# Kernel optimization log

Hardware: AMD Instinct MI355X
Metric: run time of the kernel (lower is better)

The kernel has to match this reference:

```python
import jax, jax.numpy as jnp
import numpy as np

B, N, K, F, E = 2, 16384, 32, 64, 16


def setup_inputs() -> dict:
    key = jax.random.key(0)
    k1, k2, k3, k4 = jax.random.split(key, 4)
    nodes = jax.random.normal(k1, (B, N, F), dtype=jnp.float32)
    # neighbor list: for each (batch, node) a list of K neighbor node indices
    nlist = jax.random.randint(k2, (B, N, K), 0, N, dtype=jnp.int32)
    edges = jax.random.normal(k3, (B, N, K, E), dtype=jnp.float32)
    # learned weight: (node_feat, node_feat, edge_feat) as in build()
    w = jax.random.normal(k4, (F, F, E), dtype=jnp.float32) * 0.05
    return {"nodes": nodes, "nlist": nlist, "edges": edges, "w": w}


def reference(nodes, nlist, edges, w):
    # tf.gather_nd(nodes, nlist): gather neighbor features -> [B, N, K, F]
    batch_idx = jnp.arange(nodes.shape[0], dtype=nlist.dtype)[:, None, None]
    sliced = nodes[batch_idx, nlist]  # [B, N, K, F]
    # edge-conditioned contraction: edges[b,i,j,n] * sliced[b,i,j,l] * w[l,m,n]
    prod = jnp.einsum('bijn,bijl,lmn->bijm', edges, sliced, w)  # [B, N, K, F]
    # mean over the K neighbors (axis=2); activation is None
    reduced = jnp.mean(prod, axis=2)  # [B, N, F]
    return reduced
```

## Files before the change

kernel.cpp:

```cpp
#include <hip/hip_runtime.h>
#include <cstdint>
#include <cstddef>

#define LOGN 14

typedef __bf16 bf16x8 __attribute__((ext_vector_type(8)));
typedef float f32x4 __attribute__((ext_vector_type(4)));
typedef unsigned u32;

#define BARRIER() __builtin_amdgcn_s_barrier()
#define LGKM0()   __builtin_amdgcn_s_waitcnt(0xC07F)
#define SFENCE()  __builtin_amdgcn_sched_barrier(0)

__device__ __forceinline__ u32 fbits(float f) { return __builtin_bit_cast(u32, f); }
__device__ __forceinline__ u32 pkrne(float lo, float hi) {
  u32 a = fbits(lo); a = a + 0x7fffu + ((a >> 16) & 1u);
  u32 b = fbits(hi); b = b + 0x7fffu + ((b >> 16) & 1u);
  return (b & 0xffff0000u) | (a >> 16);
}

__global__ void prep_wt(const float* __restrict__ w, unsigned short* __restrict__ wt) {
  int idx = blockIdx.x * 256 + threadIdx.x;
  int m = idx >> 10, k = idx & 1023, l = k >> 4, n = k & 15;
  u32 u = fbits(w[l * 1024 + m * 16 + n] * 0.03125f);
  wt[idx] = (unsigned short)((u + 0x7fffu + ((u >> 16) & 1u)) >> 16);
}

__device__ __forceinline__ bf16x8 mk_bw(const float* wp) {
  float v[8];
  #pragma unroll
  for (int i = 0; i < 8; ++i) v[i] = wp[i] * 0.03125f;
  uint4 pk{pkrne(v[0], v[1]), pkrne(v[2], v[3]), pkrne(v[4], v[5]), pkrne(v[6], v[7])};
  return __builtin_bit_cast(bf16x8, pk);
}

template <bool USE_WT>
__global__ __launch_bounds__(256, 3)
void mp_kernel(const float* __restrict__ nodes, const int* __restrict__ nlist,
               const float* __restrict__ edges, const unsigned short* __restrict__ wt,
               const float* __restrict__ w, float* __restrict__ out) {
  __shared__ u32 g_lds[16 * 512];

  const int tid = threadIdx.x;
  const int lane = tid & 63;
  const int wid = __builtin_amdgcn_readfirstlane(tid >> 6);
  const int q = lane >> 4, c = lane & 15;

  const int blk = blockIdx.x;
  const int xcd = blk & 7;
  const int batch = xcd >> 2;
  const int ordinal = ((blk >> 3) << 2) + (xcd & 3);
  const int wg0 = (batch << LOGN) + (ordinal << 4);
  const float* __restrict__ nbase = nodes + ((size_t)batch << 20);

  const int nd0 = wid << 2;

  auto issue_nl = [&](int t, int4* ni) {
    const int* r = nlist + (((size_t)(wg0 + nd0 + t)) << 5) + (q << 3);
    ni[0] = *(const int4*)r;
    ni[1] = *(const int4*)(r + 4);
  };
  auto issue_se = [&](int t, const int4* ni, float* S, float* E) {
    const int ix[8] = {ni[0].x, ni[0].y, ni[0].z, ni[0].w,
                       ni[1].x, ni[1].y, ni[1].z, ni[1].w};
    #pragma unroll
    for (int i = 0; i < 8; ++i) {
      const float* rp = nbase + ((size_t)(u32)ix[i] << 6) + c;
      #pragma unroll
      for (int lt = 0; lt < 4; ++lt) S[i * 4 + lt] = rp[lt << 4];
    }
    const float* ep = edges + (((size_t)(wg0 + nd0 + t)) << 9) + (q << 7) + c;
    #pragma unroll
    for (int i = 0; i < 8; ++i) E[i] = ep[i << 4];
  };
  auto consume = [&](int p, const float* S, const float* E) {
    uint4 apk{pkrne(E[0], E[1]), pkrne(E[2], E[3]),
              pkrne(E[4], E[5]), pkrne(E[6], E[7])};
    const bf16x8 af = __builtin_bit_cast(bf16x8, apk);
    #pragma unroll
    for (int lt = 0; lt < 4; ++lt) {
      uint4 spk{pkrne(S[0 * 4 + lt], S[1 * 4 + lt]),
                pkrne(S[2 * 4 + lt], S[3 * 4 + lt]),
                pkrne(S[4 * 4 + lt], S[5 * 4 + lt]),
                pkrne(S[6 * 4 + lt], S[7 * 4 + lt])};
      f32x4 acc{0.f, 0.f, 0.f, 0.f};
      acc = __builtin_amdgcn_mfma_f32_16x16x32_bf16(af,
              __builtin_bit_cast(bf16x8, spk), acc, 0, 0, 0);
      const u32 lo = pkrne(acc[0], acc[1]);
      const u32 hi = pkrne(acc[2], acc[3]);
      const int chunk = ((((lt << 4) + c) << 1) + (q >> 1)) ^ (p & 7);
      *(uint2*)&g_lds[(p << 9) + (chunk << 2) + ((q & 1) << 1)] = uint2{lo, hi};
    }
  };

  {
    int4 ni0[2], ni1[2];
    float S0[32], E0[8], S1[32], E1[8];
    issue_nl(0, ni0);
    issue_nl(1, ni1);
    issue_se(0, ni0, S0, E0);
    issue_nl(2, ni0);
    issue_se(1, ni1, S1, E1);
    issue_nl(3, ni1);
    SFENCE();
    consume(nd0 + 0, S0, E0);
    issue_se(2, ni0, S0, E0);
    SFENCE();
    consume(nd0 + 1, S1, E1);
    issue_se(3, ni1, S1, E1);
    SFENCE();
    consume(nd0 + 2, S0, E0);
    consume(nd0 + 3, S1, E1);
  }

  LGKM0();
  BARRIER();

  const int m = (wid << 4) + c;
  f32x4 ob{0.f, 0.f, 0.f, 0.f};
  if (USE_WT) {
    const unsigned short* wb = wt + ((size_t)m << 10) + (q << 3);
    #pragma unroll 8
    for (int s = 0; s < 32; ++s) {
      uint4 ar = *(const uint4*)&g_lds[(c << 9) + ((((s << 2) + q) ^ (c & 7)) << 2)];
      ob = __builtin_amdgcn_mfma_f32_16x16x32_bf16(__builtin_bit_cast(bf16x8, ar),
                                                   *(const bf16x8*)(wb + (s << 5)),
                                                   ob, 0, 0, 0);
    }
  } else {
    #pragma unroll 4
    for (int s = 0; s < 32; ++s) {
      uint4 ar = *(const uint4*)&g_lds[(c << 9) + ((((s << 2) + q) ^ (c & 7)) << 2)];
      const int l = 2 * s + (q >> 1);
      const float* wp = w + l * 1024 + m * 16 + ((q & 1) << 3);
      ob = __builtin_amdgcn_mfma_f32_16x16x32_bf16(__builtin_bit_cast(bf16x8, ar),
                                                   mk_bw(wp), ob, 0, 0, 0);
    }
  }

  #pragma unroll
  for (int r = 0; r < 4; ++r)
    out[((size_t)(wg0 + (q << 2) + r) << 6) + m] = ob[r];
}

extern "C" void kernel_launch(void* const* d_in, const int* in_sizes, int n_in,
                              void* d_out, int out_size, void* d_ws, size_t ws_size,
                              hipStream_t stream) {
  const float* nodes = (const float*)d_in[0];
  const int*   nlist = (const int*)d_in[1];
  const float* edges = (const float*)d_in[2];
  const float* w     = (const float*)d_in[3];
  float* out = (float*)d_out;

  if (ws_size >= 131072) {
    unsigned short* wt = (unsigned short*)d_ws;
    prep_wt<<<256, 256, 0, stream>>>(w, wt);
    mp_kernel<true><<<2048, 256, 0, stream>>>(nodes, nlist, edges, wt, w, out);
  } else {
    mp_kernel<false><<<2048, 256, 0, stream>>>(nodes, nlist, edges, nullptr, w, out);
  }
}
```

Measured before the change: 147.6 us.

## Vectorize neighbor feature gather to float4 and permute feature-to-lane mapping

Each lane now loads four contiguous features per neighbor with a single 16-byte load, replacing four strided scalar loads per neighbor. This changes which feature index each lane owns, so the LDS chunk layout of the intermediate and the weight reordering in both the prep kernel and the fallback path are permuted to match. The aim is fewer, wider gather loads with better coalescing per row, at the cost of a more intricate index mapping that has to stay consistent across all three places.

Measured after the change: 148.1 us. Within noise of the previous version (+0.3%).

```diff
diff --git a/kernel.cpp b/kernel.cpp
--- a/kernel.cpp
+++ b/kernel.cpp
@@ -19,9 +19,12 @@
   return (b & 0xffff0000u) | (a >> 16);
 }
 
+
 __global__ void prep_wt(const float* __restrict__ w, unsigned short* __restrict__ wt) {
   int idx = blockIdx.x * 256 + threadIdx.x;
-  int m = idx >> 10, k = idx & 1023, l = k >> 4, n = k & 15;
+  int m = idx >> 10, k = idx & 1023;
+  int ch = k >> 3, wv = k & 7, t = ch >> 4, cc = ch & 15;
+  int l = (cc << 2) + (t >> 1), n = ((t & 1) << 3) + wv;
   u32 u = fbits(w[l * 1024 + m * 16 + n] * 0.03125f);
   wt[idx] = (unsigned short)((u + 0x7fffu + ((u >> 16) & 1u)) >> 16);
 }
@@ -60,57 +63,53 @@
     ni[0] = *(const int4*)r;
     ni[1] = *(const int4*)(r + 4);
   };
-  auto issue_se = [&](int t, const int4* ni, float* S, float* E) {
+  auto issue_se = [&](int t, const int4* ni, f32x4* R, float* E) {
     const int ix[8] = {ni[0].x, ni[0].y, ni[0].z, ni[0].w,
                        ni[1].x, ni[1].y, ni[1].z, ni[1].w};
     #pragma unroll
-    for (int i = 0; i < 8; ++i) {
-      const float* rp = nbase + ((size_t)(u32)ix[i] << 6) + c;
-      #pragma unroll
-      for (int lt = 0; lt < 4; ++lt) S[i * 4 + lt] = rp[lt << 4];
-    }
+    for (int i = 0; i < 8; ++i)
+      R[i] = *(const f32x4*)(nbase + ((size_t)(u32)ix[i] << 6) + (c << 2));
     const float* ep = edges + (((size_t)(wg0 + nd0 + t)) << 9) + (q << 7) + c;
     #pragma unroll
     for (int i = 0; i < 8; ++i) E[i] = ep[i << 4];
   };
-  auto consume = [&](int p, const float* S, const float* E) {
+  auto consume = [&](int p, const f32x4* R, const float* E) {
     uint4 apk{pkrne(E[0], E[1]), pkrne(E[2], E[3]),
               pkrne(E[4], E[5]), pkrne(E[6], E[7])};
     const bf16x8 af = __builtin_bit_cast(bf16x8, apk);
     #pragma unroll
     for (int lt = 0; lt < 4; ++lt) {
-      uint4 spk{pkrne(S[0 * 4 + lt], S[1 * 4 + lt]),
-                pkrne(S[2 * 4 + lt], S[3 * 4 + lt]),
-                pkrne(S[4 * 4 + lt], S[5 * 4 + lt]),
-                pkrne(S[6 * 4 + lt], S[7 * 4 + lt])};
+      uint4 spk{pkrne(R[0][lt], R[1][lt]), pkrne(R[2][lt], R[3][lt]),
+                pkrne(R[4][lt], R[5][lt]), pkrne(R[6][lt], R[7][lt])};
       f32x4 acc{0.f, 0.f, 0.f, 0.f};
       acc = __builtin_amdgcn_mfma_f32_16x16x32_bf16(af,
               __builtin_bit_cast(bf16x8, spk), acc, 0, 0, 0);
       const u32 lo = pkrne(acc[0], acc[1]);
       const u32 hi = pkrne(acc[2], acc[3]);
-      const int chunk = ((((lt << 4) + c) << 1) + (q >> 1)) ^ (p & 7);
+      const int chunk = (c + (((lt << 1) + (q >> 1)) << 4)) ^ (p & 7);
       *(uint2*)&g_lds[(p << 9) + (chunk << 2) + ((q & 1) << 1)] = uint2{lo, hi};
     }
   };
 
   {
     int4 ni0[2], ni1[2];
-    float S0[32], E0[8], S1[32], E1[8];
+    f32x4 R0[8], R1[8];
+    float E0[8], E1[8];
     issue_nl(0, ni0);
     issue_nl(1, ni1);
-    issue_se(0, ni0, S0, E0);
+    issue_se(0, ni0, R0, E0);
     issue_nl(2, ni0);
-    issue_se(1, ni1, S1, E1);
+    issue_se(1, ni1, R1, E1);
     issue_nl(3, ni1);
     SFENCE();
-    consume(nd0 + 0, S0, E0);
-    issue_se(2, ni0, S0, E0);
+    consume(nd0 + 0, R0, E0);
+    issue_se(2, ni0, R0, E0);
     SFENCE();
-    consume(nd0 + 1, S1, E1);
-    issue_se(3, ni1, S1, E1);
+    consume(nd0 + 1, R1, E1);
+    issue_se(3, ni1, R1, E1);
     SFENCE();
-    consume(nd0 + 2, S0, E0);
-    consume(nd0 + 3, S1, E1);
+    consume(nd0 + 2, R0, E0);
+    consume(nd0 + 3, R1, E1);
   }
 
   LGKM0();
@@ -131,8 +130,10 @@
     #pragma unroll 4
     for (int s = 0; s < 32; ++s) {
       uint4 ar = *(const uint4*)&g_lds[(c << 9) + ((((s << 2) + q) ^ (c & 7)) << 2)];
-      const int l = 2 * s + (q >> 1);
-      const float* wp = w + l * 1024 + m * 16 + ((q & 1) << 3);
+      const int ch = (s << 2) + q;
+      const int l = ((ch & 15) << 2) + (ch >> 5);
+      const int n0 = ((ch >> 4) & 1) << 3;
+      const float* wp = w + l * 1024 + m * 16 + n0;
       ob = __builtin_amdgcn_mfma_f32_16x16x32_bf16(__builtin_bit_cast(bf16x8, ar),
                                                    mk_bw(wp), ob, 0, 0, 0);
     }
```
